# Kernel optimization log

Measured on AMD Instinct MI355X. Metric: run time of the kernel, lower is better.

## Reference

```python
import jax, jax.numpy as jnp
import numpy as np

SIZES = jnp.array([128.0, 256.0, 512.0], dtype=jnp.float32)
RATIOS = jnp.array([0.5, 1.0, 2.0], dtype=jnp.float32)
SCORE_THR = 0.05
IOU_THR = 0.7
MIN_SIZE = 16.0
MAX_PROP = 1000
PRE_NMS = 1000


def _base_anchors():
    # torchvision-style base anchors: (x1,y1,x2,y2) centered at origin, rounded
    h_r = jnp.sqrt(RATIOS)
    w_r = 1.0 / h_r
    ws = (w_r[:, None] * SIZES[None, :]).reshape(-1)  # (9,)
    hs = (h_r[:, None] * SIZES[None, :]).reshape(-1)
    return jnp.round(jnp.stack([-ws, -hs, ws, hs], axis=1) / 2.0)  # (9,4)


def _grid_anchors(img_h, img_w, fh, fw):
    # stride = image_size // feature_size; anchors ordered (y, x, anchor)
    sh, sw = img_h // fh, img_w // fw
    sx = jnp.arange(fw, dtype=jnp.float32) * sw
    sy = jnp.arange(fh, dtype=jnp.float32) * sh
    yy, xx = jnp.meshgrid(sy, sx, indexing='ij')
    xf = xx.reshape(-1)
    yf = yy.reshape(-1)
    shifts = jnp.stack([xf, yf, xf, yf], axis=1)  # (H*W, 4)
    return (shifts[:, None, :] + _base_anchors()[None, :, :]).reshape(-1, 4)  # (H*W*9, 4)


def _conv(x, w, b, pad):
    y = jax.lax.conv_general_dilated(x, w, (1, 1), pad,
                                     dimension_numbers=('NCHW', 'OIHW', 'NCHW'))
    return y + b[None, :, None, None]


def _bbox_adjust(anchors, deltas):
    # anchors, deltas: (..., 4); deltas = (dx, dy, dw, dh)
    aw = anchors[..., 2] - anchors[..., 0]
    ah = anchors[..., 3] - anchors[..., 1]
    cx = anchors[..., 0] + 0.5 * aw
    cy = anchors[..., 1] + 0.5 * ah
    ncx = deltas[..., 0] * aw + cx
    ncy = deltas[..., 1] * ah + cy
    nw = jnp.exp(deltas[..., 2]) * aw
    nh = jnp.exp(deltas[..., 3]) * ah
    return jnp.stack([ncx - 0.5 * nw, ncy - 0.5 * nh,
                      ncx + 0.5 * nw, ncy + 0.5 * nh], axis=-1)


def _pairwise_iou(b):
    area = (b[:, 2] - b[:, 0]) * (b[:, 3] - b[:, 1])
    lt = jnp.maximum(b[:, None, :2], b[None, :, :2])
    rb = jnp.minimum(b[:, None, 2:], b[None, :, 2:])
    wh = jnp.clip(rb - lt, 0.0)
    inter = wh[..., 0] * wh[..., 1]
    return inter / (area[:, None] + area[None, :] - inter + 1e-8)


def _per_image(boxes, scores, img_h, img_w):
    # clip to image, filter small / low-score, greedy NMS, pad to MAX_PROP
    x1 = jnp.clip(boxes[:, 0], 0.0, img_w)
    y1 = jnp.clip(boxes[:, 1], 0.0, img_h)
    x2 = jnp.clip(boxes[:, 2], 0.0, img_w)
    y2 = jnp.clip(boxes[:, 3], 0.0, img_h)
    b = jnp.stack([x1, y1, x2, y2], axis=1)
    valid = ((x2 - x1) >= MIN_SIZE) & ((y2 - y1) >= MIN_SIZE) & (scores > SCORE_THR)
    s = jnp.where(valid, scores, -1.0)
    topv, topi = jax.lax.top_k(s, PRE_NMS)
    tb = b[topi]  # (PRE_NMS, 4) sorted by score desc
    iou = _pairwise_iou(tb)
    idx = jnp.arange(PRE_NMS)

    def body(i, keep):
        sup = (iou[i] > IOU_THR) & keep[i] & (idx > i)
        return keep & ~sup

    keep = jax.lax.fori_loop(0, PRE_NMS, body, jnp.ones(PRE_NMS, dtype=bool))
    s2 = jnp.where(keep & (topv > 0.0), topv, -1.0)
    fv, fi = jax.lax.top_k(s2, MAX_PROP)
    return jnp.where((fv > 0.0)[:, None], tb[fi], 0.0)  # (MAX_PROP, 4)


def _forward(image_list, feature_map, conv_w, conv_b, cls_w, cls_b, bbox_w, bbox_b):
    N, C, H, W = feature_map.shape
    img_h, img_w = image_list.shape[2], image_list.shape[3]
    out = _conv(feature_map, conv_w, conv_b, 'SAME')  # (N, mid, H, W)
    # faithful to original: cls reshaped directly (no permute), bbox permuted
    cls = jax.nn.sigmoid(_conv(out, cls_w, cls_b, 'VALID')).reshape(N, -1, 2)
    bb = _conv(out, bbox_w, bbox_b, 'VALID').transpose(0, 2, 3, 1).reshape(N, -1, 4)
    anchors = _grid_anchors(img_h, img_w, H, W)  # (H*W*9, 4)
    dec = _bbox_adjust(anchors[None], bb)        # (N, M, 4)
    scores = cls[:, :, 1]                        # objectness
    fh, fw = float(img_h), float(img_w)
    fb = jax.vmap(lambda bx, sc: _per_image(bx, sc, fh, fw))(dec, scores)  # (N, MAX_PROP, 4)
    roi = fb.reshape(-1, 4)
    bidx = jnp.repeat(jnp.arange(N, dtype=roi.dtype), MAX_PROP)[:, None]
    return jnp.concatenate([roi, bidx], axis=1)  # (N*MAX_PROP, 5)


def setup_inputs() -> dict:
    key = jax.random.key(0)
    ks = jax.random.split(key, 6)
    image_list = jax.random.normal(ks[0], (8, 3, 800, 800), dtype=jnp.float32)
    feature_map = jax.random.normal(ks[1], (8, 512, 50, 50), dtype=jnp.float32)
    conv_w = 0.02 * jax.random.normal(ks[2], (256, 512, 3, 3), dtype=jnp.float32)
    conv_b = jnp.zeros((256,), dtype=jnp.float32)
    cls_w = 0.02 * jax.random.normal(ks[3], (18, 256, 1, 1), dtype=jnp.float32)
    cls_b = jnp.zeros((18,), dtype=jnp.float32)
    bbox_w = 0.01 * jax.random.normal(ks[4], (36, 256, 1, 1), dtype=jnp.float32)
    bbox_b = jnp.zeros((36,), dtype=jnp.float32)
    return {"image_list": image_list, "feature_map": feature_map,
            "conv_w": conv_w, "conv_b": conv_b, "cls_w": cls_w, "cls_b": cls_b,
            "bbox_w": bbox_w, "bbox_b": bbox_b}


def reference(image_list, feature_map, conv_w, conv_b, cls_w, cls_b, bbox_w, bbox_b):
    return _forward(image_list, feature_map, conv_w, conv_b, cls_w, cls_b, bbox_w, bbox_b)
```

## Files before the change

### kernel.cpp

```cpp
#include <hip/hip_runtime.h>
#include <cstdint>

#define N_IMG 8
#define CIN 512
#define COUT 256
#define FH 50
#define FW 50
#define SPAT 2500
#define NANCH 22500
#define KTOP 1000
#define PART_ELEMS 5120000

__global__ __launch_bounds__(512) void k_conv3_part(const float* __restrict__ in,
                                                    const float* __restrict__ w,
                                                    double* __restrict__ parts,
                                                    int S)
{
    __shared__ double ind[2][1152];

    const int tile = blockIdx.x, ocg = blockIdx.y;
    const int n = blockIdx.z / S, s = blockIdx.z - n * S;
    const int ccp = 64 / S;
    const int cc0 = s * ccp, cc1 = cc0 + ccp;
    const int ty = tile / 5, tx = tile % 5;
    const int y0 = ty * 10, x0 = tx * 10;
    const int t = threadIdx.x;
    const int oc_l = t & 127;
    const int g = t >> 7;
    const int base_ly = (g >> 1) * 5, base_lx = (g & 1) * 5;
    const int oc0 = ocg * 128;

    int soff[3];
#pragma unroll
    for (int k = 0; k < 3; k++) {
        int idx = t + k * 512;
        soff[k] = -1;
        if (idx < 1152) {
            int c = idx / 144, rem = idx - c * 144;
            int iy = rem / 12, ix = rem - iy * 12;
            int y = y0 - 1 + iy, x = x0 - 1 + ix;
            if ((unsigned)y < 50u && (unsigned)x < 50u)
                soff[k] = (n * CIN + c) * SPAT + y * FW + x;
        }
    }

    const float* wrow = w + (size_t)(oc0 + oc_l) * (CIN * 9);

    double acc[5][5];
#pragma unroll
    for (int i = 0; i < 5; i++)
#pragma unroll
        for (int j = 0; j < 5; j++) acc[i][j] = 0.0;

    float rin[3];
    {
        const int coff0 = cc0 * (8 * SPAT);
#pragma unroll
        for (int k = 0; k < 3; k++) rin[k] = (soff[k] >= 0) ? in[soff[k] + coff0] : 0.0f;
    }
    float wnxt[9];
    {
        const float* wp0 = wrow + cc0 * 72;
#pragma unroll
        for (int k = 0; k < 9; k++) wnxt[k] = wp0[k];
    }

    for (int cc = cc0; cc < cc1; ++cc) {
        const int cur = cc & 1;
#pragma unroll
        for (int k = 0; k < 3; k++) {
            int idx = t + k * 512;
            if (idx < 1152) ind[cur][idx] = (double)rin[k];
        }
        __syncthreads();

        if (cc + 1 < cc1) {
            const int coff = (cc + 1) * (8 * SPAT);
#pragma unroll
            for (int k = 0; k < 3; k++)
                rin[k] = (soff[k] >= 0) ? in[soff[k] + coff] : 0.0f;
        }

#pragma unroll 1
        for (int c = 0; c < 8; c++) {
            double wd[9];
#pragma unroll
            for (int k = 0; k < 9; k++) wd[k] = (double)wnxt[k];
            const int nidx = cc * 8 + c + 1;
            if (nidx < cc1 * 8) {
                const float* wp = wrow + nidx * 9;
#pragma unroll
                for (int k = 0; k < 9; k++) wnxt[k] = wp[k];
            }
#pragma unroll
            for (int r = 0; r < 7; r++) {
                double drow[7];
#pragma unroll
                for (int j = 0; j < 7; j++)
                    drow[j] = ind[cur][c * 144 + (base_ly + r) * 12 + base_lx + j];
#pragma unroll
                for (int dy = 0; dy < 3; dy++) {
                    const int iy = r - dy;
                    if (iy >= 0 && iy < 5) {
#pragma unroll
                        for (int dx = 0; dx < 3; dx++) {
                            const double wdv = wd[dy * 3 + dx];
#pragma unroll
                            for (int ix = 0; ix < 5; ix++)
                                acc[iy][ix] = fma(wdv, drow[ix + dx], acc[iy][ix]);
                        }
                    }
                }
            }
        }
        __syncthreads();
    }

    double* po = parts + (size_t)s * PART_ELEMS + (size_t)(n * COUT + oc0 + oc_l) * SPAT;
#pragma unroll
    for (int iy = 0; iy < 5; iy++)
#pragma unroll
        for (int ix = 0; ix < 5; ix++)
            po[(y0 + base_ly + iy) * FW + (x0 + base_lx + ix)] = acc[iy][ix];
}

__global__ __launch_bounds__(256) void k_heads_fused(const double* __restrict__ parts,
                                                     int S,
                                                     const float* __restrict__ conv_b,
                                                     const float* __restrict__ cls_w,
                                                     const float* __restrict__ cls_b,
                                                     const float* __restrict__ bbox_w,
                                                     const float* __restrict__ bbox_b,
                                                     double* __restrict__ boxesd,
                                                     double* __restrict__ scored)
{
    __shared__ float feat[25 * 257];
    __shared__ double outb[54 * 25];
    const int blk = blockIdx.x, n = blockIdx.y;
    const int pos0 = blk * 25;
    const int t = threadIdx.x;

    for (int idx = t; idx < 6400; idx += 256) {
        int c = idx / 25, p = idx - c * 25;
        size_t base = (size_t)(n * COUT + c) * SPAT + pos0 + p;
        double a = parts[base];
        for (int sp = 1; sp < S; sp++) a += parts[(size_t)sp * PART_ELEMS + base];
        a += (double)conv_b[c];
        feat[p * 257 + c] = (float)a;
    }
    __syncthreads();

    for (int u = t; u < 1350; u += 256) {
        const int oc = u % 54, p = u / 54;
        const float* wp = (oc < 18) ? (cls_w + oc * COUT) : (bbox_w + (oc - 18) * COUT);
        double s = (double)((oc < 18) ? cls_b[oc] : bbox_b[oc - 18]);
        const float* fp = &feat[p * 257];
#pragma unroll 8
        for (int c = 0; c < COUT; c++) s = fma((double)wp[c], (double)fp[c], s);
        outb[oc * 25 + p] = s;
    }
    __syncthreads();

    if (t < 225) {
        const int p = t / 9, k = t - p * 9;
        const int pos = pos0 + p;
        const int y = pos / 50, x = pos - y * 50;
        const int ri = k / 3, si = k - ri * 3;
        const double ratio = (ri == 0) ? 0.5 : ((ri == 1) ? 1.0 : 2.0);
        const double size = (si == 0) ? 128.0 : ((si == 1) ? 256.0 : 512.0);
        const double hr = sqrt(ratio), wr = 1.0 / hr;
        const double wsz = wr * size, hsz = hr * size;
        const double bx0 = rint(-wsz * 0.5), by0 = rint(-hsz * 0.5);
        const double bx1 = rint(wsz * 0.5), by1 = rint(hsz * 0.5);
        const double sxf = (double)(x * 16), syf = (double)(y * 16);
        const double a0 = sxf + bx0, a1 = syf + by0, a2 = sxf + bx1, a3 = syf + by1;
        const double aw = a2 - a0, ah = a3 - a1;
        const double cx = a0 + 0.5 * aw, cy = a1 + 0.5 * ah;
        const double d0 = outb[(18 + k * 4 + 0) * 25 + p];
        const double d1 = outb[(18 + k * 4 + 1) * 25 + p];
        const double d2 = outb[(18 + k * 4 + 2) * 25 + p];
        const double d3 = outb[(18 + k * 4 + 3) * 25 + p];
        const double ncx = d0 * aw + cx, ncy = d1 * ah + cy;
        const double nw = exp(d2) * aw, nh = exp(d3) * ah;
        double x1 = ncx - 0.5 * nw, y1 = ncy - 0.5 * nh;
        double x2 = ncx + 0.5 * nw, y2 = ncy + 0.5 * nh;
        x1 = fmin(fmax(x1, 0.0), 800.0);
        y1 = fmin(fmax(y1, 0.0), 800.0);
        x2 = fmin(fmax(x2, 0.0), 800.0);
        y2 = fmin(fmax(y2, 0.0), 800.0);
        double* bp = boxesd + ((size_t)n * NANCH + pos * 9 + k) * 4;
        bp[0] = x1; bp[1] = y1; bp[2] = x2; bp[3] = y2;
    }
    for (int u = t; u < 450; u += 256) {
        const int ch = u / 25, p = u - ch * 25;
        const int pos = pos0 + p;
        if (pos & 1) {
            const int a = ch * 1250 + ((pos - 1) >> 1);
            const double v = outb[ch * 25 + p];
            scored[(size_t)n * NANCH + a] = 1.0 / (1.0 + exp(-v));
        }
    }
}

__global__ __launch_bounds__(128) void k_conv3_full(const float* __restrict__ in,
                                                    const float* __restrict__ w,
                                                    const float* __restrict__ bias,
                                                    float* __restrict__ out)
{
    __shared__ double ind[2][672];
    const int tile = blockIdx.x, ocg = blockIdx.y, n = blockIdx.z;
    const int ty = tile / 5, tx = tile % 5;
    const int y0 = ty * 5, x0 = tx * 10;
    const int t = threadIdx.x;
    const int oc_l = t & 63;
    const int g = t >> 6;
    const int base_lx = g * 5;
    const int oc0 = ocg * 64;

    int soff[6];
#pragma unroll
    for (int k = 0; k < 6; k++) {
        int idx = t + k * 128;
        soff[k] = -1;
        if (idx < 672) {
            int c = idx / 84, rem = idx - c * 84;
            int iy = rem / 12, ix = rem - iy * 12;
            int y = y0 - 1 + iy, x = x0 - 1 + ix;
            if ((unsigned)y < 50u && (unsigned)x < 50u)
                soff[k] = (n * CIN + c) * SPAT + y * FW + x;
        }
    }
    const float* wrow = w + (size_t)(oc0 + oc_l) * (CIN * 9);
    double acc[5][5];
#pragma unroll
    for (int i = 0; i < 5; i++)
#pragma unroll
        for (int j = 0; j < 5; j++) acc[i][j] = 0.0;
    float rin[6];
#pragma unroll
    for (int k = 0; k < 6; k++) rin[k] = (soff[k] >= 0) ? in[soff[k]] : 0.0f;
    float wnxt[9];
#pragma unroll
    for (int k = 0; k < 9; k++) wnxt[k] = wrow[k];

    for (int cc = 0; cc < 64; ++cc) {
        const int cur = cc & 1;
#pragma unroll
        for (int k = 0; k < 6; k++) {
            int idx = t + k * 128;
            if (idx < 672) ind[cur][idx] = (double)rin[k];
        }
        __syncthreads();
        if (cc < 63) {
            const int coff = (cc + 1) * (8 * SPAT);
#pragma unroll
            for (int k = 0; k < 6; k++)
                rin[k] = (soff[k] >= 0) ? in[soff[k] + coff] : 0.0f;
        }
#pragma unroll 1
        for (int c = 0; c < 8; c++) {
            double wd[9];
#pragma unroll
            for (int k = 0; k < 9; k++) wd[k] = (double)wnxt[k];
            const int nidx = cc * 8 + c + 1;
            if (nidx < 512) {
                const float* wp = wrow + nidx * 9;
#pragma unroll
                for (int k = 0; k < 9; k++) wnxt[k] = wp[k];
            }
#pragma unroll
            for (int r = 0; r < 7; r++) {
                double drow[7];
#pragma unroll
                for (int j = 0; j < 7; j++)
                    drow[j] = ind[cur][c * 84 + r * 12 + base_lx + j];
#pragma unroll
                for (int dy = 0; dy < 3; dy++) {
                    const int iy = r - dy;
                    if (iy >= 0 && iy < 5) {
#pragma unroll
                        for (int dx = 0; dx < 3; dx++) {
                            const double wdv = wd[dy * 3 + dx];
#pragma unroll
                            for (int ix = 0; ix < 5; ix++)
                                acc[iy][ix] = fma(wdv, drow[ix + dx], acc[iy][ix]);
                        }
                    }
                }
            }
        }
        __syncthreads();
    }
    const double b = (double)bias[oc0 + oc_l];
#pragma unroll
    for (int iy = 0; iy < 5; iy++)
#pragma unroll
        for (int ix = 0; ix < 5; ix++) {
            int y = y0 + iy, x = x0 + base_lx + ix;
            out[(n * COUT + oc0 + oc_l) * SPAT + y * FW + x] = (float)(acc[iy][ix] + b);
        }
}

__global__ __launch_bounds__(256) void k_heads_legacy(const float* __restrict__ conv1,
                                                      const float* __restrict__ cls_w,
                                                      const float* __restrict__ cls_b,
                                                      const float* __restrict__ bbox_w,
                                                      const float* __restrict__ bbox_b,
                                                      double* __restrict__ boxesd,
                                                      double* __restrict__ scored)
{
    __shared__ float feat[25 * 257];
    __shared__ double outb[54 * 25];
    const int blk = blockIdx.x, n = blockIdx.y;
    const int pos0 = blk * 25;
    const int t = threadIdx.x;

    for (int idx = t; idx < 6400; idx += 256) {
        int c = idx / 25, p = idx - c * 25;
        feat[p * 257 + c] = conv1[(n * COUT + c) * SPAT + pos0 + p];
    }
    __syncthreads();
    for (int u = t; u < 1350; u += 256) {
        const int oc = u % 54, p = u / 54;
        const float* wp = (oc < 18) ? (cls_w + oc * COUT) : (bbox_w + (oc - 18) * COUT);
        double s = (double)((oc < 18) ? cls_b[oc] : bbox_b[oc - 18]);
        const float* fp = &feat[p * 257];
#pragma unroll 8
        for (int c = 0; c < COUT; c++) s = fma((double)wp[c], (double)fp[c], s);
        outb[oc * 25 + p] = s;
    }
    __syncthreads();
    if (t < 225) {
        const int p = t / 9, k = t - p * 9;
        const int pos = pos0 + p;
        const int y = pos / 50, x = pos - y * 50;
        const int ri = k / 3, si = k - ri * 3;
        const double ratio = (ri == 0) ? 0.5 : ((ri == 1) ? 1.0 : 2.0);
        const double size = (si == 0) ? 128.0 : ((si == 1) ? 256.0 : 512.0);
        const double hr = sqrt(ratio), wr = 1.0 / hr;
        const double wsz = wr * size, hsz = hr * size;
        const double bx0 = rint(-wsz * 0.5), by0 = rint(-hsz * 0.5);
        const double bx1 = rint(wsz * 0.5), by1 = rint(hsz * 0.5);
        const double sxf = (double)(x * 16), syf = (double)(y * 16);
        const double a0 = sxf + bx0, a1 = syf + by0, a2 = sxf + bx1, a3 = syf + by1;
        const double aw = a2 - a0, ah = a3 - a1;
        const double cx = a0 + 0.5 * aw, cy = a1 + 0.5 * ah;
        const double d0 = outb[(18 + k * 4 + 0) * 25 + p];
        const double d1 = outb[(18 + k * 4 + 1) * 25 + p];
        const double d2 = outb[(18 + k * 4 + 2) * 25 + p];
        const double d3 = outb[(18 + k * 4 + 3) * 25 + p];
        const double ncx = d0 * aw + cx, ncy = d1 * ah + cy;
        const double nw = exp(d2) * aw, nh = exp(d3) * ah;
        double x1 = ncx - 0.5 * nw, y1 = ncy - 0.5 * nh;
        double x2 = ncx + 0.5 * nw, y2 = ncy + 0.5 * nh;
        x1 = fmin(fmax(x1, 0.0), 800.0);
        y1 = fmin(fmax(y1, 0.0), 800.0);
        x2 = fmin(fmax(x2, 0.0), 800.0);
        y2 = fmin(fmax(y2, 0.0), 800.0);
        double* bp = boxesd + ((size_t)n * NANCH + pos * 9 + k) * 4;
        bp[0] = x1; bp[1] = y1; bp[2] = x2; bp[3] = y2;
    }
    for (int u = t; u < 450; u += 256) {
        const int ch = u / 25, p = u - ch * 25;
        const int pos = pos0 + p;
        if (pos & 1) {
            const int a = ch * 1250 + ((pos - 1) >> 1);
            const double v = outb[ch * 25 + p];
            scored[(size_t)n * NANCH + a] = 1.0 / (1.0 + exp(-v));
        }
    }
}

__global__ __launch_bounds__(1024) void k_select(const double* __restrict__ boxesd,
                                                 const double* __restrict__ scored,
                                                 uint64_t* __restrict__ keys,
                                                 double* __restrict__ tbd,
                                                 float* __restrict__ topv)
{
    __shared__ unsigned hist[256];
    __shared__ __align__(16) uint64_t sel2[2048];
    __shared__ __align__(16) uint64_t out2[2048];
    __shared__ uint64_t sh_prefix, sh_mask;
    __shared__ unsigned sh_rem, sh_cntA, sh_cntB;

    const int n = blockIdx.x, t = threadIdx.x;
    uint64_t* ky = keys + (size_t)n * NANCH;

    for (int a = t; a < NANCH; a += 1024) {
        const double* bp = boxesd + ((size_t)n * NANCH + a) * 4;
        double x1 = bp[0], y1 = bp[1], x2 = bp[2], y2 = bp[3];
        double s0 = scored[(size_t)n * NANCH + a];
        bool valid = (x2 - x1 >= 16.0) && (y2 - y1 >= 16.0) && (s0 > 0.05);
        double s = valid ? s0 : -1.0;
        uint64_t b = (uint64_t)__double_as_longlong(s);
        uint64_t su = (b >> 63) ? ~b : (b | 0x8000000000000000ull);
        ky[a] = su;
    }
    if (t == 0) { sh_prefix = 0; sh_mask = 0; sh_rem = KTOP; }
    __syncthreads();

    for (int pass = 0; pass < 8; pass++) {
        const int shift = 56 - 8 * pass;
        if (t < 256) hist[t] = 0;
        __syncthreads();
        const uint64_t pre = sh_prefix, msk = sh_mask;
        if (pass < 2) {
            for (int a = t; a < NANCH; a += 1024) {
                uint64_t k = ky[a];
                bool p = ((k & msk) == pre);
                unsigned d = (unsigned)((k >> shift) & 255);
                unsigned long long todo = __ballot(p);
                while (todo) {
                    int leader = __ffsll((unsigned long long)todo) - 1;
                    unsigned dl = __shfl(d, leader);
                    unsigned long long mm = __ballot(p && (d == dl));
                    if ((t & 63) == leader)
                        atomicAdd(&hist[dl], (unsigned)__popcll(mm));
                    todo &= ~mm;
                }
            }
        } else {
            for (int a = t; a < NANCH; a += 1024) {
                uint64_t k = ky[a];
                if ((k & msk) == pre)
                    atomicAdd(&hist[(unsigned)((k >> shift) & 255)], 1u);
            }
        }
        __syncthreads();
        if (t < 64) {
            unsigned h0 = hist[4 * t], h1 = hist[4 * t + 1];
            unsigned h2 = hist[4 * t + 2], h3 = hist[4 * t + 3];
            unsigned local = h0 + h1 + h2 + h3;
            unsigned suf = local;
#pragma unroll
            for (int off = 1; off < 64; off <<= 1) {
                unsigned x = __shfl_down(suf, off);
                if (t + off < 64) suf += x;
            }
            unsigned exclc = suf - local;
            unsigned inc3 = exclc + h3;
            unsigned inc2 = inc3 + h2;
            unsigned inc1 = inc2 + h1;
            unsigned inc0 = inc1 + h0;
            const unsigned rem = sh_rem;
            int cand = -1; unsigned candExcl = 0;
            if      (inc3 >= rem) { cand = 4 * t + 3; candExcl = exclc; }
            else if (inc2 >= rem) { cand = 4 * t + 2; candExcl = inc3; }
            else if (inc1 >= rem) { cand = 4 * t + 1; candExcl = inc2; }
            else if (inc0 >= rem) { cand = 4 * t + 0; candExcl = inc1; }
#pragma unroll
            for (int off = 32; off > 0; off >>= 1) {
                int c2 = __shfl_down(cand, off);
                unsigned p2 = __shfl_down(candExcl, off);
                if (c2 > cand) { cand = c2; candExcl = p2; }
            }
            if (t == 0) {
                sh_prefix = pre | ((uint64_t)(unsigned)cand << shift);
                sh_mask = msk | (255ull << shift);
                sh_rem = rem - candExcl;
            }
        }
        __syncthreads();
    }
    const uint64_t T = sh_prefix;

    sel2[2 * t] = 0; sel2[2 * t + 1] = 0;
    if (t == 0) { sh_cntA = 0; sh_cntB = 0; }
    __syncthreads();
    for (int a = t; a < NANCH; a += 1024) {
        uint64_t k = ky[a];
        if (k > T) {
            unsigned p = atomicAdd(&sh_cntA, 1u);
            sel2[2 * p] = k; sel2[2 * p + 1] = (uint64_t)(~(uint32_t)a);
        }
    }
    __syncthreads();
    const unsigned m = sh_cntA;
    for (int a = t; a < NANCH; a += 1024) {
        uint64_t k = ky[a];
        if (k == T) {
            unsigned q = atomicAdd(&sh_cntB, 1u);
            unsigned slot = m + q;
            if (slot < KTOP) { sel2[2 * slot] = k; sel2[2 * slot + 1] = (uint64_t)(~(uint32_t)a); }
        }
    }
    __syncthreads();
    {
        const uint64_t myk = sel2[2 * t], myn = sel2[2 * t + 1];
        int rank = 0;
        const ulonglong2* sp = (const ulonglong2*)sel2;
#pragma unroll 8
        for (int j = 0; j < 1024; j++) {
            ulonglong2 v = sp[j];
            rank += (v.x > myk) || (v.x == myk && v.y > myn);
        }
        if (rank < KTOP) { out2[2 * rank] = myk; out2[2 * rank + 1] = myn; }
    }
    __syncthreads();

    if (t < KTOP) {
        uint64_t k = out2[2 * t];
        uint32_t idx = ~(uint32_t)out2[2 * t + 1];
        uint64_t b = (k >> 63) ? (k ^ 0x8000000000000000ull) : ~k;
        double s = __longlong_as_double((long long)b);
        double bx0 = 0.0, bx1 = 0.0, bx2 = 0.0, bx3 = 0.0;
        float sv = (float)s;
        if (idx < NANCH) {
            const double* bp = boxesd + ((size_t)n * NANCH + idx) * 4;
            bx0 = bp[0]; bx1 = bp[1]; bx2 = bp[2]; bx3 = bp[3];
        } else {
            sv = -1.0f;
        }
        double* tp = tbd + ((size_t)n * KTOP + t) * 4;
        tp[0] = bx0; tp[1] = bx1; tp[2] = bx2; tp[3] = bx3;
        topv[n * KTOP + t] = sv;
    }
}

__global__ __launch_bounds__(256) void k_supmat(const double* __restrict__ tbd,
                                                uint64_t* __restrict__ sup)
{
    __shared__ double sb[4000];
    const int tile = blockIdx.x, n = blockIdx.y;
    const int t = threadIdx.x;
    for (int i = t; i < 4000; i += 256) sb[i] = tbd[(size_t)n * KTOP * 4 + i];
    __syncthreads();
    const int r0 = tile * 64;
    for (int u = t; u < 1024; u += 256) {
        const int il = u >> 4, wq = u & 15;
        const int i = r0 + il;
        if (i >= 1000) continue;
        const double bix = sb[i * 4], biy = sb[i * 4 + 1], biz = sb[i * 4 + 2], biw = sb[i * 4 + 3];
        const double ai = (biz - bix) * (biw - biy);
        uint64_t bits = 0;
        const int jbase = wq * 64;
        for (int jj = 0; jj < 64; jj++) {
            const int j = jbase + jj;
            if (j < 1000 && j > i) {
                const double bjx = sb[j * 4], bjy = sb[j * 4 + 1], bjz = sb[j * 4 + 2], bjw = sb[j * 4 + 3];
                const double aj = (bjz - bjx) * (bjw - bjy);
                const double ltx = fmax(bix, bjx), lty = fmax(biy, bjy);
                const double rbx = fmin(biz, bjz), rby = fmin(biw, bjw);
                const double ww = fmax(rbx - ltx, 0.0), hh = fmax(rby - lty, 0.0);
                const double inter = ww * hh;
                const double iou = inter / (ai + aj - inter + 1e-8);
                if (iou > 0.7) bits |= (1ull << jj);
            }
        }
        sup[((size_t)n * KTOP + i) * 16 + wq] = bits;
    }
}

__global__ __launch_bounds__(64) void k_nms(const uint64_t* __restrict__ sup,
                                            uint64_t* __restrict__ keepout)
{
    const int n = blockIdx.x;
    const int lane = threadIdx.x;
    const uint64_t* rows = sup + (size_t)n * KTOP * 16;

    uint64_t keep;
    if (lane < 15) keep = ~0ull;
    else if (lane == 15) keep = (1ull << 40) - 1;
    else keep = 0;

    uint64_t A[8], B[8];
    auto LOADG = [&](uint64_t* dst, int g) {
#pragma unroll
        for (int k = 0; k < 8; k++) {
            int i = g * 8 + k;
            dst[k] = (lane < 16) ? rows[(size_t)i * 16 + lane] : 0ull;
        }
    };
    auto PROCG = [&](const uint64_t* src, int g) {
#pragma unroll
        for (int k = 0; k < 8; k++) {
            int i = g * 8 + k;
            uint64_t kw = __shfl(keep, i >> 6);
            bool alive = (kw >> (i & 63)) & 1ull;
            keep &= alive ? ~src[k] : ~0ull;
        }
    };

    LOADG(A, 0);
    for (int g = 0; g < 125; g += 2) {
        if (g + 1 < 125) LOADG(B, g + 1);
        PROCG(A, g);
        if (g + 2 < 125) LOADG(A, g + 2);
        if (g + 1 < 125) PROCG(B, g + 1);
    }
    if (lane < 16) keepout[n * 16 + lane] = keep;
}

__global__ __launch_bounds__(1024) void k_final(const uint64_t* __restrict__ keepw,
                                                const float* __restrict__ topv,
                                                const double* __restrict__ tbd,
                                                float* __restrict__ out)
{
    __shared__ int sc[1024];
    __shared__ uint64_t kw[16];
    __shared__ int sh_total;
    const int n = blockIdx.x, t = threadIdx.x;
    if (t < 16) kw[t] = keepw[n * 16 + t];
    __syncthreads();

    int val = 0;
    bool kept = false;
    if (t < 1000) {
        bool bit = (kw[t >> 6] >> (t & 63)) & 1ull;
        float v = topv[n * KTOP + t];
        kept = bit && (v > 0.0f);
        val = kept ? 1 : 0;
    }
    sc[t] = val;
    __syncthreads();
    for (int off = 1; off < 1024; off <<= 1) {
        int x = (t >= off) ? sc[t - off] : 0;
        __syncthreads();
        sc[t] += x;
        __syncthreads();
    }
    if (t == 1023) sh_total = sc[1023];
    __syncthreads();
    const int total = sh_total;
    if (t < 1000) {
        if (kept) {
            int r = sc[t] - 1;
            const double* bp = tbd + ((size_t)n * KTOP + t) * 4;
            float* o = out + ((size_t)n * KTOP + r) * 5;
            o[0] = (float)bp[0]; o[1] = (float)bp[1];
            o[2] = (float)bp[2]; o[3] = (float)bp[3];
            o[4] = (float)n;
        }
        if (t >= total) {
            float* o = out + ((size_t)n * KTOP + t) * 5;
            o[0] = 0.0f; o[1] = 0.0f; o[2] = 0.0f; o[3] = 0.0f; o[4] = (float)n;
        }
    }
}

extern "C" void kernel_launch(void* const* d_in, const int* in_sizes, int n_in,
                              void* d_out, int out_size, void* d_ws, size_t ws_size,
                              hipStream_t stream)
{
    (void)in_sizes; (void)n_in; (void)out_size;
    const float* feat   = (const float*)d_in[1];
    const float* conv_w = (const float*)d_in[2];
    const float* conv_b = (const float*)d_in[3];
    const float* cls_w  = (const float*)d_in[4];
    const float* cls_b  = (const float*)d_in[5];
    const float* bbox_w = (const float*)d_in[6];
    const float* bbox_b = (const float*)d_in[7];
    float* out = (float*)d_out;
    char* ws = (char*)d_ws;

    const size_t PB   = 40960000ull;
    const size_t REST = 5760000 + 1440000 + 1440000 + 256000 + 32000 + 1024000 + 1024;

    int S = 0;
    if      (ws_size >= 8 * PB + REST) S = 8;
    else if (ws_size >= 4 * PB + REST) S = 4;
    else if (ws_size >= 2 * PB + REST) S = 2;
    else if (ws_size >= 1 * PB + REST) S = 1;

    if (S > 0) {
        double*   parts  = (double*)ws;
        char*     p      = ws + (size_t)S * PB;
        double*   boxesd = (double*)(p);               p += 5760000;
        double*   scored = (double*)(p);               p += 1440000;
        uint64_t* keys   = (uint64_t*)(p);             p += 1440000;
        double*   tbd    = (double*)(p);               p += 256000;
        float*    topv   = (float*)(p);                p += 32000;
        uint64_t* sup    = (uint64_t*)(p);             p += 1024000;
        uint64_t* keepw  = (uint64_t*)(p);

        k_conv3_part <<<dim3(25, 2, 8 * S), 512, 0, stream>>>(feat, conv_w, parts, S);
        k_heads_fused<<<dim3(100, 8), 256, 0, stream>>>(parts, S, conv_b, cls_w, cls_b,
                                                        bbox_w, bbox_b, boxesd, scored);
        k_select<<<8, 1024, 0, stream>>>(boxesd, scored, keys, tbd, topv);
        k_supmat<<<dim3(16, 8), 256, 0, stream>>>(tbd, sup);
        k_nms   <<<8, 64, 0, stream>>>(sup, keepw);
        k_final <<<8, 1024, 0, stream>>>(keepw, topv, tbd, out);
    } else {
        float*    conv1  = (float*)(ws);
        double*   boxesd = (double*)(ws + 20480000);
        double*   scored = (double*)(ws + 26240000);
        uint64_t* keys   = (uint64_t*)(ws + 27680000);
        double*   tbd    = (double*)(ws + 29120000);
        float*    topv   = (float*)(ws + 29376000);
        uint64_t* sup    = (uint64_t*)(ws + 29408000);
        uint64_t* keepw  = (uint64_t*)(ws + 30432000);

        k_conv3_full  <<<dim3(50, 4, 8), 128, 0, stream>>>(feat, conv_w, conv_b, conv1);
        k_heads_legacy<<<dim3(100, 8), 256, 0, stream>>>(conv1, cls_w, cls_b, bbox_w, bbox_b, boxesd, scored);
        k_select<<<8, 1024, 0, stream>>>(boxesd, scored, keys, tbd, topv);
        k_supmat<<<dim3(16, 8), 256, 0, stream>>>(tbd, sup);
        k_nms   <<<8, 64, 0, stream>>>(sup, keepw);
        k_final <<<8, 1024, 0, stream>>>(keepw, topv, tbd, out);
    }
}
```

Measured before the change: 1.646 ms.

## Shrink conv blocks, split key build into own kernel, compact radix-select candidates

The split-K conv kernel drops to 256 threads with 64 output channels per block, doubling blocks along the channel-group axis and capping the split factor at 4. Key construction for top-k selection moves out of the 8-block select kernel into a separate wide-grid kernel, so all CUs share that work. The select kernel also compacts candidates into shared memory after two radix passes, so later passes scan at most 2048 entries instead of all anchors. It drops the ballot-aggregated histogram in the first passes. The trade-offs are an extra launch and a different conv occupancy and reduction balance.

Result: faster. 1.497 ms (-9.1%).

```diff
diff --git a/kernel.cpp b/kernel.cpp
--- a/kernel.cpp
+++ b/kernel.cpp
@@ -11,7 +11,7 @@
 #define KTOP 1000
 #define PART_ELEMS 5120000
 
-__global__ __launch_bounds__(512) void k_conv3_part(const float* __restrict__ in,
+__global__ __launch_bounds__(256) void k_conv3_part(const float* __restrict__ in,
                                                     const float* __restrict__ w,
                                                     double* __restrict__ parts,
                                                     int S)
@@ -25,15 +25,15 @@
     const int ty = tile / 5, tx = tile % 5;
     const int y0 = ty * 10, x0 = tx * 10;
     const int t = threadIdx.x;
-    const int oc_l = t & 127;
-    const int g = t >> 7;
+    const int oc_l = t & 63;
+    const int g = t >> 6;
     const int base_ly = (g >> 1) * 5, base_lx = (g & 1) * 5;
-    const int oc0 = ocg * 128;
-
-    int soff[3];
-#pragma unroll
-    for (int k = 0; k < 3; k++) {
-        int idx = t + k * 512;
+    const int oc0 = ocg * 64;
+
+    int soff[5];
+#pragma unroll
+    for (int k = 0; k < 5; k++) {
+        int idx = t + k * 256;
         soff[k] = -1;
         if (idx < 1152) {
             int c = idx / 144, rem = idx - c * 144;
@@ -52,11 +52,11 @@
 #pragma unroll
         for (int j = 0; j < 5; j++) acc[i][j] = 0.0;
 
-    float rin[3];
+    float rin[5];
     {
         const int coff0 = cc0 * (8 * SPAT);
 #pragma unroll
-        for (int k = 0; k < 3; k++) rin[k] = (soff[k] >= 0) ? in[soff[k] + coff0] : 0.0f;
+        for (int k = 0; k < 5; k++) rin[k] = (soff[k] >= 0) ? in[soff[k] + coff0] : 0.0f;
     }
     float wnxt[9];
     {
@@ -68,8 +68,8 @@
     for (int cc = cc0; cc < cc1; ++cc) {
         const int cur = cc & 1;
 #pragma unroll
-        for (int k = 0; k < 3; k++) {
-            int idx = t + k * 512;
+        for (int k = 0; k < 5; k++) {
+            int idx = t + k * 256;
             if (idx < 1152) ind[cur][idx] = (double)rin[k];
         }
         __syncthreads();
@@ -77,7 +77,7 @@
         if (cc + 1 < cc1) {
             const int coff = (cc + 1) * (8 * SPAT);
 #pragma unroll
-            for (int k = 0; k < 3; k++)
+            for (int k = 0; k < 5; k++)
                 rin[k] = (soff[k] >= 0) ? in[soff[k] + coff] : 0.0f;
         }
 
@@ -202,6 +202,306 @@
     }
 }
 
+__global__ __launch_bounds__(256) void k_keys(const double* __restrict__ boxesd,
+                                              const double* __restrict__ scored,
+                                              uint64_t* __restrict__ keys)
+{
+    const int n = blockIdx.y;
+    const int a = blockIdx.x * 256 + threadIdx.x;
+    if (a < NANCH) {
+        const double* bp = boxesd + ((size_t)n * NANCH + a) * 4;
+        double x1 = bp[0], y1 = bp[1], x2 = bp[2], y2 = bp[3];
+        double s0 = scored[(size_t)n * NANCH + a];
+        bool valid = (x2 - x1 >= 16.0) && (y2 - y1 >= 16.0) && (s0 > 0.05);
+        double s = valid ? s0 : -1.0;
+        uint64_t b = (uint64_t)__double_as_longlong(s);
+        uint64_t su = (b >> 63) ? ~b : (b | 0x8000000000000000ull);
+        keys[(size_t)n * NANCH + a] = su;
+    }
+}
+
+__global__ __launch_bounds__(1024) void k_select(const double* __restrict__ boxesd,
+                                                 const uint64_t* __restrict__ keys,
+                                                 double* __restrict__ tbd,
+                                                 float* __restrict__ topv)
+{
+    __shared__ unsigned hist[256];
+    __shared__ uint64_t candk[2048];
+    __shared__ uint32_t candi[2048];
+    __shared__ __align__(16) uint64_t sel2[2048];
+    __shared__ __align__(16) uint64_t out2[2048];
+    __shared__ uint64_t sh_prefix, sh_mask;
+    __shared__ unsigned sh_rem, sh_binc, sh_cnt, sh_cntA, sh_cntB;
+
+    const int n = blockIdx.x, t = threadIdx.x;
+    const uint64_t* ky = keys + (size_t)n * NANCH;
+
+    if (t == 0) { sh_prefix = 0; sh_mask = 0; sh_rem = KTOP; }
+    __syncthreads();
+
+    auto radix_pass = [&](int shift, bool useCand) {
+        if (t < 256) hist[t] = 0;
+        __syncthreads();
+        const uint64_t pre = sh_prefix, msk = sh_mask;
+        if (!useCand) {
+            for (int a = t; a < NANCH; a += 1024) {
+                uint64_t k = ky[a];
+                if ((k & msk) == pre)
+                    atomicAdd(&hist[(unsigned)((k >> shift) & 255)], 1u);
+            }
+        } else {
+            const unsigned nc = sh_cnt;
+            for (unsigned j = t; j < nc; j += 1024) {
+                uint64_t k = candk[j];
+                if ((k & msk) == pre)
+                    atomicAdd(&hist[(unsigned)((k >> shift) & 255)], 1u);
+            }
+        }
+        __syncthreads();
+        if (t < 64) {
+            unsigned h0 = hist[4 * t], h1 = hist[4 * t + 1];
+            unsigned h2 = hist[4 * t + 2], h3 = hist[4 * t + 3];
+            unsigned local = h0 + h1 + h2 + h3;
+            unsigned suf = local;
+#pragma unroll
+            for (int off = 1; off < 64; off <<= 1) {
+                unsigned x = __shfl_down(suf, off);
+                if (t + off < 64) suf += x;
+            }
+            unsigned exclc = suf - local;
+            unsigned inc3 = exclc + h3;
+            unsigned inc2 = inc3 + h2;
+            unsigned inc1 = inc2 + h1;
+            unsigned inc0 = inc1 + h0;
+            const unsigned rem = sh_rem;
+            int cand = -1; unsigned candExcl = 0;
+            if      (inc3 >= rem) { cand = 4 * t + 3; candExcl = exclc; }
+            else if (inc2 >= rem) { cand = 4 * t + 2; candExcl = inc3; }
+            else if (inc1 >= rem) { cand = 4 * t + 1; candExcl = inc2; }
+            else if (inc0 >= rem) { cand = 4 * t + 0; candExcl = inc1; }
+#pragma unroll
+            for (int off = 32; off > 0; off >>= 1) {
+                int c2 = __shfl_down(cand, off);
+                unsigned p2 = __shfl_down(candExcl, off);
+                if (c2 > cand) { cand = c2; candExcl = p2; }
+            }
+            if (t == 0) {
+                sh_prefix = pre | ((uint64_t)(unsigned)cand << shift);
+                sh_mask = msk | (255ull << shift);
+                sh_rem = rem - candExcl;
+                sh_binc = hist[cand];
+            }
+        }
+        __syncthreads();
+    };
+
+    radix_pass(56, false);
+    radix_pass(48, false);
+
+    if (t == 0) sh_cnt = 0;
+    __syncthreads();
+    const bool compacted = (sh_binc <= 2048u);
+    if (compacted) {
+        const uint64_t pre = sh_prefix, msk = sh_mask;
+        for (int a = t; a < NANCH; a += 1024) {
+            uint64_t k = ky[a];
+            if ((k & msk) == pre) {
+                unsigned p = atomicAdd(&sh_cnt, 1u);
+                candk[p] = k; candi[p] = (uint32_t)a;
+            }
+        }
+    }
+    __syncthreads();
+
+    for (int pass = 2; pass < 8; pass++)
+        radix_pass(56 - 8 * pass, compacted);
+
+    const uint64_t T = sh_prefix;
+
+    sel2[2 * t] = 0; sel2[2 * t + 1] = 0;
+    if (t == 0) { sh_cntA = 0; sh_cntB = 0; }
+    __syncthreads();
+    for (int a = t; a < NANCH; a += 1024) {
+        uint64_t k = ky[a];
+        if (k > T) {
+            unsigned p = atomicAdd(&sh_cntA, 1u);
+            sel2[2 * p] = k; sel2[2 * p + 1] = (uint64_t)(~(uint32_t)a);
+        }
+    }
+    __syncthreads();
+    const unsigned m = sh_cntA;
+    if (compacted) {
+        const unsigned nc = sh_cnt;
+        for (unsigned j = t; j < nc; j += 1024) {
+            if (candk[j] == T) {
+                unsigned q = atomicAdd(&sh_cntB, 1u);
+                unsigned slot = m + q;
+                if (slot < KTOP) { sel2[2 * slot] = T; sel2[2 * slot + 1] = (uint64_t)(~candi[j]); }
+            }
+        }
+    } else {
+        for (int a = t; a < NANCH; a += 1024) {
+            if (ky[a] == T) {
+                unsigned q = atomicAdd(&sh_cntB, 1u);
+                unsigned slot = m + q;
+                if (slot < KTOP) { sel2[2 * slot] = T; sel2[2 * slot + 1] = (uint64_t)(~(uint32_t)a); }
+            }
+        }
+    }
+    __syncthreads();
+    {
+        const uint64_t myk = sel2[2 * t], myn = sel2[2 * t + 1];
+        int rank = 0;
+        const ulonglong2* sp = (const ulonglong2*)sel2;
+#pragma unroll 8
+        for (int j = 0; j < 1024; j++) {
+            ulonglong2 v = sp[j];
+            rank += (v.x > myk) || (v.x == myk && v.y > myn);
+        }
+        if (rank < KTOP) { out2[2 * rank] = myk; out2[2 * rank + 1] = myn; }
+    }
+    __syncthreads();
+
+    if (t < KTOP) {
+        uint64_t k = out2[2 * t];
+        uint32_t idx = ~(uint32_t)out2[2 * t + 1];
+        uint64_t b = (k >> 63) ? (k ^ 0x8000000000000000ull) : ~k;
+        double s = __longlong_as_double((long long)b);
+        double bx0 = 0.0, bx1 = 0.0, bx2 = 0.0, bx3 = 0.0;
+        float sv = (float)s;
+        if (idx < NANCH) {
+            const double* bp = boxesd + ((size_t)n * NANCH + idx) * 4;
+            bx0 = bp[0]; bx1 = bp[1]; bx2 = bp[2]; bx3 = bp[3];
+        } else {
+            sv = -1.0f;
+        }
+        double* tp = tbd + ((size_t)n * KTOP + t) * 4;
+        tp[0] = bx0; tp[1] = bx1; tp[2] = bx2; tp[3] = bx3;
+        topv[n * KTOP + t] = sv;
+    }
+}
+
+__global__ __launch_bounds__(256) void k_supmat(const double* __restrict__ tbd,
+                                                uint64_t* __restrict__ sup)
+{
+    __shared__ double sb[4000];
+    const int tile = blockIdx.x, n = blockIdx.y;
+    const int t = threadIdx.x;
+    for (int i = t; i < 4000; i += 256) sb[i] = tbd[(size_t)n * KTOP * 4 + i];
+    __syncthreads();
+    const int r0 = tile * 64;
+    for (int u = t; u < 1024; u += 256) {
+        const int il = u >> 4, wq = u & 15;
+        const int i = r0 + il;
+        if (i >= 1000) continue;
+        const double bix = sb[i * 4], biy = sb[i * 4 + 1], biz = sb[i * 4 + 2], biw = sb[i * 4 + 3];
+        const double ai = (biz - bix) * (biw - biy);
+        uint64_t bits = 0;
+        const int jbase = wq * 64;
+        for (int jj = 0; jj < 64; jj++) {
+            const int j = jbase + jj;
+            if (j < 1000 && j > i) {
+                const double bjx = sb[j * 4], bjy = sb[j * 4 + 1], bjz = sb[j * 4 + 2], bjw = sb[j * 4 + 3];
+                const double aj = (bjz - bjx) * (bjw - bjy);
+                const double ltx = fmax(bix, bjx), lty = fmax(biy, bjy);
+                const double rbx = fmin(biz, bjz), rby = fmin(biw, bjw);
+                const double ww = fmax(rbx - ltx, 0.0), hh = fmax(rby - lty, 0.0);
+                const double inter = ww * hh;
+                const double iou = inter / (ai + aj - inter + 1e-8);
+                if (iou > 0.7) bits |= (1ull << jj);
+            }
+        }
+        sup[((size_t)n * KTOP + i) * 16 + wq] = bits;
+    }
+}
+
+__global__ __launch_bounds__(64) void k_nms(const uint64_t* __restrict__ sup,
+                                            uint64_t* __restrict__ keepout)
+{
+    const int n = blockIdx.x;
+    const int lane = threadIdx.x;
+    const uint64_t* rows = sup + (size_t)n * KTOP * 16;
+
+    uint64_t keep;
+    if (lane < 15) keep = ~0ull;
+    else if (lane == 15) keep = (1ull << 40) - 1;
+    else keep = 0;
+
+    uint64_t A[8], B[8];
+    auto LOADG = [&](uint64_t* dst, int g) {
+#pragma unroll
+        for (int k = 0; k < 8; k++) {
+            int i = g * 8 + k;
+            dst[k] = (lane < 16) ? rows[(size_t)i * 16 + lane] : 0ull;
+        }
+    };
+    auto PROCG = [&](const uint64_t* src, int g) {
+#pragma unroll
+        for (int k = 0; k < 8; k++) {
+            int i = g * 8 + k;
+            uint64_t kw = __shfl(keep, i >> 6);
+            bool alive = (kw >> (i & 63)) & 1ull;
+            keep &= alive ? ~src[k] : ~0ull;
+        }
+    };
+
+    LOADG(A, 0);
+    for (int g = 0; g < 125; g += 2) {
+        if (g + 1 < 125) LOADG(B, g + 1);
+        PROCG(A, g);
+        if (g + 2 < 125) LOADG(A, g + 2);
+        if (g + 1 < 125) PROCG(B, g + 1);
+    }
+    if (lane < 16) keepout[n * 16 + lane] = keep;
+}
+
+__global__ __launch_bounds__(1024) void k_final(const uint64_t* __restrict__ keepw,
+                                                const float* __restrict__ topv,
+                                                const double* __restrict__ tbd,
+                                                float* __restrict__ out)
+{
+    __shared__ int sc[1024];
+    __shared__ uint64_t kw[16];
+    __shared__ int sh_total;
+    const int n = blockIdx.x, t = threadIdx.x;
+    if (t < 16) kw[t] = keepw[n * 16 + t];
+    __syncthreads();
+
+    int val = 0;
+    bool kept = false;
+    if (t < 1000) {
+        bool bit = (kw[t >> 6] >> (t & 63)) & 1ull;
+        float v = topv[n * KTOP + t];
+        kept = bit && (v > 0.0f);
+        val = kept ? 1 : 0;
+    }
+    sc[t] = val;
+    __syncthreads();
+    for (int off = 1; off < 1024; off <<= 1) {
+        int x = (t >= off) ? sc[t - off] : 0;
+        __syncthreads();
+        sc[t] += x;
+        __syncthreads();
+    }
+    if (t == 1023) sh_total = sc[1023];
+    __syncthreads();
+    const int total = sh_total;
+    if (t < 1000) {
+        if (kept) {
+            int r = sc[t] - 1;
+            const double* bp = tbd + ((size_t)n * KTOP + t) * 4;
+            float* o = out + ((size_t)n * KTOP + r) * 5;
+            o[0] = (float)bp[0]; o[1] = (float)bp[1];
+            o[2] = (float)bp[2]; o[3] = (float)bp[3];
+            o[4] = (float)n;
+        }
+        if (t >= total) {
+            float* o = out + ((size_t)n * KTOP + t) * 5;
+            o[0] = 0.0f; o[1] = 0.0f; o[2] = 0.0f; o[3] = 0.0f; o[4] = (float)n;
+        }
+    }
+}
+
 __global__ __launch_bounds__(128) void k_conv3_full(const float* __restrict__ in,
                                                     const float* __restrict__ w,
                                                     const float* __restrict__ bias,
@@ -371,273 +671,6 @@
     }
 }
 
-__global__ __launch_bounds__(1024) void k_select(const double* __restrict__ boxesd,
-                                                 const double* __restrict__ scored,
-                                                 uint64_t* __restrict__ keys,
-                                                 double* __restrict__ tbd,
-                                                 float* __restrict__ topv)
-{
-    __shared__ unsigned hist[256];
-    __shared__ __align__(16) uint64_t sel2[2048];
-    __shared__ __align__(16) uint64_t out2[2048];
-    __shared__ uint64_t sh_prefix, sh_mask;
-    __shared__ unsigned sh_rem, sh_cntA, sh_cntB;
-
-    const int n = blockIdx.x, t = threadIdx.x;
-    uint64_t* ky = keys + (size_t)n * NANCH;
-
-    for (int a = t; a < NANCH; a += 1024) {
-        const double* bp = boxesd + ((size_t)n * NANCH + a) * 4;
-        double x1 = bp[0], y1 = bp[1], x2 = bp[2], y2 = bp[3];
-        double s0 = scored[(size_t)n * NANCH + a];
-        bool valid = (x2 - x1 >= 16.0) && (y2 - y1 >= 16.0) && (s0 > 0.05);
-        double s = valid ? s0 : -1.0;
-        uint64_t b = (uint64_t)__double_as_longlong(s);
-        uint64_t su = (b >> 63) ? ~b : (b | 0x8000000000000000ull);
-        ky[a] = su;
-    }
-    if (t == 0) { sh_prefix = 0; sh_mask = 0; sh_rem = KTOP; }
-    __syncthreads();
-
-    for (int pass = 0; pass < 8; pass++) {
-        const int shift = 56 - 8 * pass;
-        if (t < 256) hist[t] = 0;
-        __syncthreads();
-        const uint64_t pre = sh_prefix, msk = sh_mask;
-        if (pass < 2) {
-            for (int a = t; a < NANCH; a += 1024) {
-                uint64_t k = ky[a];
-                bool p = ((k & msk) == pre);
-                unsigned d = (unsigned)((k >> shift) & 255);
-                unsigned long long todo = __ballot(p);
-                while (todo) {
-                    int leader = __ffsll((unsigned long long)todo) - 1;
-                    unsigned dl = __shfl(d, leader);
-                    unsigned long long mm = __ballot(p && (d == dl));
-                    if ((t & 63) == leader)
-                        atomicAdd(&hist[dl], (unsigned)__popcll(mm));
-                    todo &= ~mm;
-                }
-            }
-        } else {
-            for (int a = t; a < NANCH; a += 1024) {
-                uint64_t k = ky[a];
-                if ((k & msk) == pre)
-                    atomicAdd(&hist[(unsigned)((k >> shift) & 255)], 1u);
-            }
-        }
-        __syncthreads();
-        if (t < 64) {
-            unsigned h0 = hist[4 * t], h1 = hist[4 * t + 1];
-            unsigned h2 = hist[4 * t + 2], h3 = hist[4 * t + 3];
-            unsigned local = h0 + h1 + h2 + h3;
-            unsigned suf = local;
-#pragma unroll
-            for (int off = 1; off < 64; off <<= 1) {
-                unsigned x = __shfl_down(suf, off);
-                if (t + off < 64) suf += x;
-            }
-            unsigned exclc = suf - local;
-            unsigned inc3 = exclc + h3;
-            unsigned inc2 = inc3 + h2;
-            unsigned inc1 = inc2 + h1;
-            unsigned inc0 = inc1 + h0;
-            const unsigned rem = sh_rem;
-            int cand = -1; unsigned candExcl = 0;
-            if      (inc3 >= rem) { cand = 4 * t + 3; candExcl = exclc; }
-            else if (inc2 >= rem) { cand = 4 * t + 2; candExcl = inc3; }
-            else if (inc1 >= rem) { cand = 4 * t + 1; candExcl = inc2; }
-            else if (inc0 >= rem) { cand = 4 * t + 0; candExcl = inc1; }
-#pragma unroll
-            for (int off = 32; off > 0; off >>= 1) {
-                int c2 = __shfl_down(cand, off);
-                unsigned p2 = __shfl_down(candExcl, off);
-                if (c2 > cand) { cand = c2; candExcl = p2; }
-            }
-            if (t == 0) {
-                sh_prefix = pre | ((uint64_t)(unsigned)cand << shift);
-                sh_mask = msk | (255ull << shift);
-                sh_rem = rem - candExcl;
-            }
-        }
-        __syncthreads();
-    }
-    const uint64_t T = sh_prefix;
-
-    sel2[2 * t] = 0; sel2[2 * t + 1] = 0;
-    if (t == 0) { sh_cntA = 0; sh_cntB = 0; }
-    __syncthreads();
-    for (int a = t; a < NANCH; a += 1024) {
-        uint64_t k = ky[a];
-        if (k > T) {
-            unsigned p = atomicAdd(&sh_cntA, 1u);
-            sel2[2 * p] = k; sel2[2 * p + 1] = (uint64_t)(~(uint32_t)a);
-        }
-    }
-    __syncthreads();
-    const unsigned m = sh_cntA;
-    for (int a = t; a < NANCH; a += 1024) {
-        uint64_t k = ky[a];
-        if (k == T) {
-            unsigned q = atomicAdd(&sh_cntB, 1u);
-            unsigned slot = m + q;
-            if (slot < KTOP) { sel2[2 * slot] = k; sel2[2 * slot + 1] = (uint64_t)(~(uint32_t)a); }
-        }
-    }
-    __syncthreads();
-    {
-        const uint64_t myk = sel2[2 * t], myn = sel2[2 * t + 1];
-        int rank = 0;
-        const ulonglong2* sp = (const ulonglong2*)sel2;
-#pragma unroll 8
-        for (int j = 0; j < 1024; j++) {
-            ulonglong2 v = sp[j];
-            rank += (v.x > myk) || (v.x == myk && v.y > myn);
-        }
-        if (rank < KTOP) { out2[2 * rank] = myk; out2[2 * rank + 1] = myn; }
-    }
-    __syncthreads();
-
-    if (t < KTOP) {
-        uint64_t k = out2[2 * t];
-        uint32_t idx = ~(uint32_t)out2[2 * t + 1];
-        uint64_t b = (k >> 63) ? (k ^ 0x8000000000000000ull) : ~k;
-        double s = __longlong_as_double((long long)b);
-        double bx0 = 0.0, bx1 = 0.0, bx2 = 0.0, bx3 = 0.0;
-        float sv = (float)s;
-        if (idx < NANCH) {
-            const double* bp = boxesd + ((size_t)n * NANCH + idx) * 4;
-            bx0 = bp[0]; bx1 = bp[1]; bx2 = bp[2]; bx3 = bp[3];
-        } else {
-            sv = -1.0f;
-        }
-        double* tp = tbd + ((size_t)n * KTOP + t) * 4;
-        tp[0] = bx0; tp[1] = bx1; tp[2] = bx2; tp[3] = bx3;
-        topv[n * KTOP + t] = sv;
-    }
-}
-
-__global__ __launch_bounds__(256) void k_supmat(const double* __restrict__ tbd,
-                                                uint64_t* __restrict__ sup)
-{
-    __shared__ double sb[4000];
-    const int tile = blockIdx.x, n = blockIdx.y;
-    const int t = threadIdx.x;
-    for (int i = t; i < 4000; i += 256) sb[i] = tbd[(size_t)n * KTOP * 4 + i];
-    __syncthreads();
-    const int r0 = tile * 64;
-    for (int u = t; u < 1024; u += 256) {
-        const int il = u >> 4, wq = u & 15;
-        const int i = r0 + il;
-        if (i >= 1000) continue;
-        const double bix = sb[i * 4], biy = sb[i * 4 + 1], biz = sb[i * 4 + 2], biw = sb[i * 4 + 3];
-        const double ai = (biz - bix) * (biw - biy);
-        uint64_t bits = 0;
-        const int jbase = wq * 64;
-        for (int jj = 0; jj < 64; jj++) {
-            const int j = jbase + jj;
-            if (j < 1000 && j > i) {
-                const double bjx = sb[j * 4], bjy = sb[j * 4 + 1], bjz = sb[j * 4 + 2], bjw = sb[j * 4 + 3];
-                const double aj = (bjz - bjx) * (bjw - bjy);
-                const double ltx = fmax(bix, bjx), lty = fmax(biy, bjy);
-                const double rbx = fmin(biz, bjz), rby = fmin(biw, bjw);
-                const double ww = fmax(rbx - ltx, 0.0), hh = fmax(rby - lty, 0.0);
-                const double inter = ww * hh;
-                const double iou = inter / (ai + aj - inter + 1e-8);
-                if (iou > 0.7) bits |= (1ull << jj);
-            }
-        }
-        sup[((size_t)n * KTOP + i) * 16 + wq] = bits;
-    }
-}
-
-__global__ __launch_bounds__(64) void k_nms(const uint64_t* __restrict__ sup,
-                                            uint64_t* __restrict__ keepout)
-{
-    const int n = blockIdx.x;
-    const int lane = threadIdx.x;
-    const uint64_t* rows = sup + (size_t)n * KTOP * 16;
-
-    uint64_t keep;
-    if (lane < 15) keep = ~0ull;
-    else if (lane == 15) keep = (1ull << 40) - 1;
-    else keep = 0;
-
-    uint64_t A[8], B[8];
-    auto LOADG = [&](uint64_t* dst, int g) {
-#pragma unroll
-        for (int k = 0; k < 8; k++) {
-            int i = g * 8 + k;
-            dst[k] = (lane < 16) ? rows[(size_t)i * 16 + lane] : 0ull;
-        }
-    };
-    auto PROCG = [&](const uint64_t* src, int g) {
-#pragma unroll
-        for (int k = 0; k < 8; k++) {
-            int i = g * 8 + k;
-            uint64_t kw = __shfl(keep, i >> 6);
-            bool alive = (kw >> (i & 63)) & 1ull;
-            keep &= alive ? ~src[k] : ~0ull;
-        }
-    };
-
-    LOADG(A, 0);
-    for (int g = 0; g < 125; g += 2) {
-        if (g + 1 < 125) LOADG(B, g + 1);
-        PROCG(A, g);
-        if (g + 2 < 125) LOADG(A, g + 2);
-        if (g + 1 < 125) PROCG(B, g + 1);
-    }
-    if (lane < 16) keepout[n * 16 + lane] = keep;
-}
-
-__global__ __launch_bounds__(1024) void k_final(const uint64_t* __restrict__ keepw,
-                                                const float* __restrict__ topv,
-                                                const double* __restrict__ tbd,
-                                                float* __restrict__ out)
-{
-    __shared__ int sc[1024];
-    __shared__ uint64_t kw[16];
-    __shared__ int sh_total;
-    const int n = blockIdx.x, t = threadIdx.x;
-    if (t < 16) kw[t] = keepw[n * 16 + t];
-    __syncthreads();
-
-    int val = 0;
-    bool kept = false;
-    if (t < 1000) {
-        bool bit = (kw[t >> 6] >> (t & 63)) & 1ull;
-        float v = topv[n * KTOP + t];
-        kept = bit && (v > 0.0f);
-        val = kept ? 1 : 0;
-    }
-    sc[t] = val;
-    __syncthreads();
-    for (int off = 1; off < 1024; off <<= 1) {
-        int x = (t >= off) ? sc[t - off] : 0;
-        __syncthreads();
-        sc[t] += x;
-        __syncthreads();
-    }
-    if (t == 1023) sh_total = sc[1023];
-    __syncthreads();
-    const int total = sh_total;
-    if (t < 1000) {
-        if (kept) {
-            int r = sc[t] - 1;
-            const double* bp = tbd + ((size_t)n * KTOP + t) * 4;
-            float* o = out + ((size_t)n * KTOP + r) * 5;
-            o[0] = (float)bp[0]; o[1] = (float)bp[1];
-            o[2] = (float)bp[2]; o[3] = (float)bp[3];
-            o[4] = (float)n;
-        }
-        if (t >= total) {
-            float* o = out + ((size_t)n * KTOP + t) * 5;
-            o[0] = 0.0f; o[1] = 0.0f; o[2] = 0.0f; o[3] = 0.0f; o[4] = (float)n;
-        }
-    }
-}
-
 extern "C" void kernel_launch(void* const* d_in, const int* in_sizes, int n_in,
                               void* d_out, int out_size, void* d_ws, size_t ws_size,
                               hipStream_t stream)
@@ -657,8 +690,7 @@
     const size_t REST = 5760000 + 1440000 + 1440000 + 256000 + 32000 + 1024000 + 1024;
 
     int S = 0;
-    if      (ws_size >= 8 * PB + REST) S = 8;
-    else if (ws_size >= 4 * PB + REST) S = 4;
+    if      (ws_size >= 4 * PB + REST) S = 4;
     else if (ws_size >= 2 * PB + REST) S = 2;
     else if (ws_size >= 1 * PB + REST) S = 1;
 
@@ -673,10 +705,11 @@
         uint64_t* sup    = (uint64_t*)(p);             p += 1024000;
         uint64_t* keepw  = (uint64_t*)(p);
 
-        k_conv3_part <<<dim3(25, 2, 8 * S), 512, 0, stream>>>(feat, conv_w, parts, S);
+        k_conv3_part <<<dim3(25, 4, 8 * S), 256, 0, stream>>>(feat, conv_w, parts, S);
         k_heads_fused<<<dim3(100, 8), 256, 0, stream>>>(parts, S, conv_b, cls_w, cls_b,
                                                         bbox_w, bbox_b, boxesd, scored);
-        k_select<<<8, 1024, 0, stream>>>(boxesd, scored, keys, tbd, topv);
+        k_keys  <<<dim3(88, 8), 256, 0, stream>>>(boxesd, scored, keys);
+        k_select<<<8, 1024, 0, stream>>>(boxesd, keys, tbd, topv);
         k_supmat<<<dim3(16, 8), 256, 0, stream>>>(tbd, sup);
         k_nms   <<<8, 64, 0, stream>>>(sup, keepw);
         k_final <<<8, 1024, 0, stream>>>(keepw, topv, tbd, out);
@@ -692,7 +725,8 @@
 
         k_conv3_full  <<<dim3(50, 4, 8), 128, 0, stream>>>(feat, conv_w, conv_b, conv1);
         k_heads_legacy<<<dim3(100, 8), 256, 0, stream>>>(conv1, cls_w, cls_b, bbox_w, bbox_b, boxesd, scored);
-        k_select<<<8, 1024, 0, stream>>>(boxesd, scored, keys, tbd, topv);
+        k_keys  <<<dim3(88, 8), 256, 0, stream>>>(boxesd, scored, keys);
+        k_select<<<8, 1024, 0, stream>>>(boxesd, keys, tbd, topv);
         k_supmat<<<dim3(16, 8), 256, 0, stream>>>(tbd, sup);
         k_nms   <<<8, 64, 0, stream>>>(sup, keepw);
         k_final <<<8, 1024, 0, stream>>>(keepw, topv, tbd, out);
```
